# Kernel tuning notes

Measured on AMD Instinct MI355X. Metric: run time of the kernel, lower is better.

## Reference

```python
import jax, jax.numpy as jnp
import numpy as np
import math

B, N, M = 128, 32, 64           # batch, num_agents, num_other
OBS, ACT = 128, 16              # obs_input_dim, num_actions
D_QK = 128                      # obs_output_dim (== obs_output_dim_other)
D_AV = 64                       # obs_act_output_dim (== other)
F_IN = OBS + ACT                # obs_act_input_dim = 144


def _xavier(key, shape):
    fan_in, fan_out = shape[0], shape[1]
    limit = math.sqrt(6.0 / (fan_in + fan_out))
    return jax.random.uniform(key, shape, jnp.float32, -limit, limit)


def setup_inputs() -> dict:
    key = jax.random.key(0)
    ks = jax.random.split(key, 13)
    return {
        "states": jax.random.normal(ks[0], (B, N, OBS), jnp.float32),
        "policies": jax.random.uniform(ks[1], (B, N, ACT), jnp.float32),
        "actions": jax.random.uniform(ks[2], (B, N, ACT), jnp.float32),
        "states_other": jax.random.normal(ks[3], (B, M, OBS), jnp.float32),
        "actions_other": jax.random.uniform(ks[4], (B, M, ACT), jnp.float32),
        # weights stored as [in, out] (x @ W == nn.Linear without bias)
        "W_key": _xavier(ks[5], (OBS, D_QK)),
        "W_query": _xavier(ks[6], (OBS, D_QK)),
        "W_av": _xavier(ks[7], (F_IN, D_AV)),
        "W_key_other": _xavier(ks[8], (OBS, D_QK)),
        "W_query_other": _xavier(ks[9], (OBS, D_QK)),
        "W_av_other": _xavier(ks[10], (F_IN, D_AV)),
        "W_f1": _xavier(ks[11], (2 * D_AV, 64)),
        "W_f2": _xavier(ks[12], (64, 1)),
    }


def reference(states, policies, actions, states_other, actions_other,
              W_key, W_query, W_av, W_key_other, W_query_other,
              W_av_other, W_f1, W_f2):
    b, n, _ = states.shape
    obs_actions = jnp.concatenate([states, actions], axis=-1)   # [B,N,F_IN]
    obs_policy = jnp.concatenate([states, policies], axis=-1)   # [B,N,F_IN]

    key_obs = states @ W_key                                    # [B,N,D_QK]
    query_obs = states @ W_query                                # [B,N,D_QK]
    d_k = W_key.shape[1]
    weight = jax.nn.softmax(
        jnp.einsum('bid,bjd->bij', query_obs, key_obs) / math.sqrt(d_k), axis=-1)
    ret_weight = weight

    # place_policies is identity on (j,k): oap[b,j,k] = obs_policy[b,k] if j==k else obs_actions[b,k]
    eye = jnp.eye(n, dtype=states.dtype)[None, :, :, None]       # [1,N,N,1]
    oap = eye * obs_policy[:, None, :, :] + (1.0 - eye) * obs_actions[:, None, :, :]
    attention_values = jnp.tanh(oap @ W_av)                      # [B,N,N,D_AV] (j,k)

    # repeat-mul-sum == weighted reduction over k: wav[b,i,j,d] = sum_k w[b,i,k] av[b,j,k,d]
    wav = jnp.einsum('bik,bjkd->bijd', weight, attention_values)  # [B,N,N,D_AV]

    obs_actions_other = jnp.concatenate([states_other, actions_other], axis=-1)
    keys_other = states_other @ W_key_other                      # [B,M,D_QK]
    query_agent = states @ W_query_other                         # [B,N,D_QK]
    av_other = jnp.tanh(obs_actions_other @ W_av_other)          # [B,M,D_AV]
    d_k_o = W_key_other.shape[1]
    weight_other = jax.nn.softmax(
        jnp.einsum('bid,bmd->bim', query_agent, keys_other) / math.sqrt(d_k_o), axis=-1)
    wav_other = jnp.einsum('bim,bmd->bid', weight_other, av_other)  # [B,N,D_AV]

    # broadcast the per-agent other-branch features across the j axis for the concat
    wav_other_b = jnp.broadcast_to(wav_other[:, :, None, :], wav.shape[:-1] + (wav_other.shape[-1],))
    node_features = jnp.concatenate([wav, wav_other_b], axis=-1)  # [B,N,N,2*D_AV]

    h = jax.nn.leaky_relu(node_features @ W_f1, negative_slope=0.01)
    value = h @ W_f2                                              # [B,N,N,1]
    return value, ret_weight, weight_other
```

## Files before the change

kernel.cpp:

```cpp
#include <hip/hip_runtime.h>
#include <math.h>

#define WS_WQK    0
#define WS_WQKO   16384
#define WS_AVAPRJ 32768
#define WS_DPROJ  294912
#define WS_AVOPRJ 557056

#define INV_SQRT_DK 0.08838834764831845f

__device__ __forceinline__ float dot4(float4 a, float4 b) {
  return a.x*b.x + a.y*b.y + a.z*b.z + a.w*b.w;
}

__global__ __launch_bounds__(256) void k1_pre(
    const float* __restrict__ g_states, const float* __restrict__ g_pol,
    const float* __restrict__ g_act, const float* __restrict__ g_so,
    const float* __restrict__ g_ao,
    const float* __restrict__ Wq, const float* __restrict__ Wk,
    const float* __restrict__ Wqo, const float* __restrict__ Wko,
    const float* __restrict__ W_av, const float* __restrict__ W_avo,
    const float* __restrict__ W_f1, float* __restrict__ ws)
{
  __shared__ __align__(16) float pool[8576];
  const int t = threadIdx.x;
  int blk = blockIdx.x;

  if (blk < 32) {
    const float* A; const float* Bm; float* O;
    if (blk < 16) { A = Wq;  Bm = Wk;  O = ws + WS_WQK; }
    else          { A = Wqo; Bm = Wko; O = ws + WS_WQKO; blk -= 16; }
    const int tr = (blk >> 2) << 5;
    const int tc = (blk & 3) << 5;
    float* sA = pool;
    float* sB = pool + 4224;
    const float4* a4 = (const float4*)(A + tr * 128);
    const float4* b4 = (const float4*)(Bm + tc * 128);
    #pragma unroll
    for (int u = 0; u < 4; ++u) {
      int f = t + u * 256;
      int r = f >> 5, c4 = f & 31;
      *(float4*)(sA + r*132 + c4*4) = a4[f];
      *(float4*)(sB + r*132 + c4*4) = b4[f];
    }
    __syncthreads();
    const int e = t & 31, cl0 = t >> 5;
    float acc[4] = {0,0,0,0};
    #pragma unroll 4
    for (int d4 = 0; d4 < 32; ++d4) {
      float4 bv = *(const float4*)(sB + e*132 + d4*4);
      #pragma unroll
      for (int rr = 0; rr < 4; ++rr) {
        float4 av = *(const float4*)(sA + (cl0 + rr*8)*132 + d4*4);
        acc[rr] += dot4(av, bv);
      }
    }
    #pragma unroll
    for (int rr = 0; rr < 4; ++rr)
      O[(tr + cl0 + rr*8)*128 + tc + e] = acc[rr];
    return;
  }
  blk -= 32;

  if (blk < 128) {
    const int b = blk;
    float* s_pre = pool;
    float* s_av  = pool + 4224;
    float* s_dl  = pool + 6400;
    {
      const int wv_  = t >> 6;
      const int ap   = wv_ & 1;
      const int rh   = wv_ >> 1;
      const int lane = t & 63;
      const float* gs = g_states + b*4096 + rh*16*128;
      const float* gt = (ap ? g_pol : g_act) + b*512 + rh*16*16;
      float acc[16];
      #pragma unroll
      for (int r = 0; r < 16; ++r) acc[r] = 0.f;
      #pragma unroll 4
      for (int c4 = 0; c4 < 32; ++c4) {
        const float w0 = W_av[(c4*4+0)*64 + lane];
        const float w1 = W_av[(c4*4+1)*64 + lane];
        const float w2 = W_av[(c4*4+2)*64 + lane];
        const float w3 = W_av[(c4*4+3)*64 + lane];
        #pragma unroll
        for (int r = 0; r < 16; ++r) {
          float4 sv = *(const float4*)(gs + r*128 + c4*4);
          acc[r] += sv.x*w0 + sv.y*w1 + sv.z*w2 + sv.w*w3;
        }
      }
      #pragma unroll
      for (int c4 = 0; c4 < 4; ++c4) {
        const float w0 = W_av[(128 + c4*4+0)*64 + lane];
        const float w1 = W_av[(128 + c4*4+1)*64 + lane];
        const float w2 = W_av[(128 + c4*4+2)*64 + lane];
        const float w3 = W_av[(128 + c4*4+3)*64 + lane];
        #pragma unroll
        for (int r = 0; r < 16; ++r) {
          float4 sv = *(const float4*)(gt + r*16 + c4*4);
          acc[r] += sv.x*w0 + sv.y*w1 + sv.z*w2 + sv.w*w3;
        }
      }
      #pragma unroll
      for (int r = 0; r < 16; ++r)
        s_pre[(rh*16 + r)*132 + ap*64 + lane] = acc[r];
    }
    __syncthreads();
    {
      const int r = t >> 3, d0 = (t & 7) << 3;
      float4 a0 = *(const float4*)(s_pre + r*132 + d0);
      float4 a1 = *(const float4*)(s_pre + r*132 + d0 + 4);
      float4 p0 = *(const float4*)(s_pre + r*132 + 64 + d0);
      float4 p1 = *(const float4*)(s_pre + r*132 + 64 + d0 + 4);
      float4 va0, va1, dl0, dl1;
      va0.x = tanhf(a0.x); va0.y = tanhf(a0.y); va0.z = tanhf(a0.z); va0.w = tanhf(a0.w);
      va1.x = tanhf(a1.x); va1.y = tanhf(a1.y); va1.z = tanhf(a1.z); va1.w = tanhf(a1.w);
      dl0.x = tanhf(p0.x) - va0.x; dl0.y = tanhf(p0.y) - va0.y;
      dl0.z = tanhf(p0.z) - va0.z; dl0.w = tanhf(p0.w) - va0.w;
      dl1.x = tanhf(p1.x) - va1.x; dl1.y = tanhf(p1.y) - va1.y;
      dl1.z = tanhf(p1.z) - va1.z; dl1.w = tanhf(p1.w) - va1.w;
      *(float4*)(s_av + r*68 + d0)     = va0;
      *(float4*)(s_av + r*68 + d0 + 4) = va1;
      *(float4*)(s_dl + r*68 + d0)     = dl0;
      *(float4*)(s_dl + r*68 + d0 + 4) = dl1;
    }
    __syncthreads();
    {
      const int h = t & 63;
      const int j0 = (t >> 6) << 3;
      float da[8] = {0,0,0,0,0,0,0,0};
      float aa[8] = {0,0,0,0,0,0,0,0};
      #pragma unroll 4
      for (int d4 = 0; d4 < 16; ++d4) {
        float w0 = W_f1[(d4*4+0)*64 + h];
        float w1 = W_f1[(d4*4+1)*64 + h];
        float w2 = W_f1[(d4*4+2)*64 + h];
        float w3 = W_f1[(d4*4+3)*64 + h];
        #pragma unroll
        for (int q = 0; q < 8; ++q) {
          float4 dv = *(const float4*)(s_dl + (j0+q)*68 + d4*4);
          float4 av = *(const float4*)(s_av + (j0+q)*68 + d4*4);
          da[q] += dv.x*w0 + dv.y*w1 + dv.z*w2 + dv.w*w3;
          aa[q] += av.x*w0 + av.y*w1 + av.z*w2 + av.w*w3;
        }
      }
      #pragma unroll
      for (int q = 0; q < 8; ++q) {
        ws[WS_DPROJ  + b*2048 + (j0+q)*64 + h] = da[q];
        ws[WS_AVAPRJ + b*2048 + (j0+q)*64 + h] = aa[q];
      }
    }
    return;
  }
  blk -= 128;

  {
    const int b = blk >> 1, m0 = (blk & 1) << 5;
    float* s_avo = pool;
    const int wv_  = t >> 6;
    const int lane = t & 63;
    const float* gso = g_so + (b*64 + m0 + wv_*8) * 128;
    const float* gao = g_ao + (b*64 + m0 + wv_*8) * 16;
    float acc[8];
    #pragma unroll
    for (int r = 0; r < 8; ++r) acc[r] = 0.f;
    #pragma unroll 4
    for (int c4 = 0; c4 < 32; ++c4) {
      const float w0 = W_avo[(c4*4+0)*64 + lane];
      const float w1 = W_avo[(c4*4+1)*64 + lane];
      const float w2 = W_avo[(c4*4+2)*64 + lane];
      const float w3 = W_avo[(c4*4+3)*64 + lane];
      #pragma unroll
      for (int r = 0; r < 8; ++r) {
        float4 sv = *(const float4*)(gso + r*128 + c4*4);
        acc[r] += sv.x*w0 + sv.y*w1 + sv.z*w2 + sv.w*w3;
      }
    }
    #pragma unroll
    for (int c4 = 0; c4 < 4; ++c4) {
      const float w0 = W_avo[(128 + c4*4+0)*64 + lane];
      const float w1 = W_avo[(128 + c4*4+1)*64 + lane];
      const float w2 = W_avo[(128 + c4*4+2)*64 + lane];
      const float w3 = W_avo[(128 + c4*4+3)*64 + lane];
      #pragma unroll
      for (int r = 0; r < 8; ++r) {
        float4 sv = *(const float4*)(gao + r*16 + c4*4);
        acc[r] += sv.x*w0 + sv.y*w1 + sv.z*w2 + sv.w*w3;
      }
    }
    #pragma unroll
    for (int r = 0; r < 8; ++r)
      s_avo[(wv_*8 + r)*68 + lane] = tanhf(acc[r]);
    __syncthreads();
    {
      const int h = t & 63;
      const int j0 = (t >> 6) << 3;
      float oa[8] = {0,0,0,0,0,0,0,0};
      #pragma unroll 4
      for (int d4 = 0; d4 < 16; ++d4) {
        float w0 = W_f1[(64 + d4*4+0)*64 + h];
        float w1 = W_f1[(64 + d4*4+1)*64 + h];
        float w2 = W_f1[(64 + d4*4+2)*64 + h];
        float w3 = W_f1[(64 + d4*4+3)*64 + h];
        #pragma unroll
        for (int q = 0; q < 8; ++q) {
          float4 ov = *(const float4*)(s_avo + (j0+q)*68 + d4*4);
          oa[q] += ov.x*w0 + ov.y*w1 + ov.z*w2 + ov.w*w3;
        }
      }
      #pragma unroll
      for (int q = 0; q < 8; ++q)
        ws[WS_AVOPRJ + b*4096 + (m0 + j0 + q)*64 + h] = oa[q];
    }
  }
}

__global__ __launch_bounds__(256) void k2_main(
    const float* __restrict__ g_states, const float* __restrict__ g_so,
    const float* __restrict__ ws, float* __restrict__ out,
    const float* __restrict__ W_f2)
{
  __shared__ __align__(16) float pool[12288];
  float* s_st   = pool;
  float* s_avOp = pool;
  float* s_avAp = pool + 4352;
  float* s_dp   = pool + 6528;
  float* s_P    = pool + 8704;
  float* s_w    = pool + 10848;
  float* s_wo   = pool + 11136;
  float* s_base = pool + 11680;
  float* s_wf2  = pool + 12224;

  const int t = threadIdx.x;
  const int b = blockIdx.x >> 2;
  const int i0 = (blockIdx.x & 3) << 3;

  {
    const float4* gs4 = (const float4*)(g_states + b * 4096);
    #pragma unroll
    for (int u = 0; u < 4; ++u) {
      int f = t + u * 256;
      int r = f >> 5, c4 = f & 31;
      *(float4*)(s_st + r*132 + c4*4) = gs4[f];
    }
    #pragma unroll
    for (int u = 0; u < 2; ++u) {
      int f = t + u * 256;
      int k = f >> 4, dq = f & 15;
      *(float4*)(s_avAp + k*68 + dq*4) = ((const float4*)(ws + WS_AVAPRJ + b*2048))[f];
      *(float4*)(s_dp   + k*68 + dq*4) = ((const float4*)(ws + WS_DPROJ  + b*2048))[f];
    }
    if (t < 16) *(float4*)(s_wf2 + t*4) = ((const float4*)W_f2)[t];
  }

  {
    const int wv_ = t >> 6, lane = t & 63;
    const int cg  = wv_*64 + lane;
    const float* Wp = (wv_ < 2) ? (ws + WS_WQK  + cg)
                                : (ws + WS_WQKO + cg - 128);
    const float* srow = g_states + b*4096 + i0*128;
    float acc[8] = {0,0,0,0,0,0,0,0};
    #pragma unroll 4
    for (int c4 = 0; c4 < 32; ++c4) {
      float4 sv[8];
      #pragma unroll
      for (int r = 0; r < 8; ++r)
        sv[r] = *(const float4*)(srow + r*128 + c4*4);
      #pragma unroll
      for (int kk = 0; kk < 4; ++kk) {
        float wv = Wp[(c4*4 + kk)*128];
        #pragma unroll
        for (int r = 0; r < 8; ++r)
          acc[r] += wv * ((const float*)&sv[r])[kk];
      }
    }
    #pragma unroll
    for (int r = 0; r < 8; ++r)
      s_P[r*268 + cg] = acc[r];
  }
  __syncthreads();

  {
    const int r = t >> 5, j = t & 31;
    float acc = 0.f;
    #pragma unroll 8
    for (int e4 = 0; e4 < 32; ++e4) {
      float4 p4  = *(const float4*)(s_P + r*268 + e4*4);
      float4 st4 = *(const float4*)(s_st + j*132 + e4*4);
      acc += dot4(p4, st4);
    }
    acc *= INV_SQRT_DK;
    float mx = acc;
    for (int off = 16; off; off >>= 1) mx = fmaxf(mx, __shfl_xor(mx, off, 32));
    float ev = __expf(acc - mx);
    float sum = ev;
    for (int off = 16; off; off >>= 1) sum += __shfl_xor(sum, off, 32);
    float wn = ev / sum;
    out[131072 + b*1024 + (i0 + r)*32 + j] = wn;
    s_w[r*36 + j] = wn;
  }
  __syncthreads();

  for (int tt = 0; tt < 2; ++tt) {
    const float4* gt4 = (const float4*)(g_so + (b*64 + tt*32) * 128);
    #pragma unroll
    for (int u = 0; u < 4; ++u) {
      int f = t + u * 256;
      int r = f >> 5, c4 = f & 31;
      *(float4*)(s_st + r*132 + c4*4) = gt4[f];
    }
    __syncthreads();
    const int r = t >> 5, m = t & 31;
    float acc = 0.f;
    #pragma unroll 8
    for (int c4 = 0; c4 < 32; ++c4) {
      float4 p4  = *(const float4*)(s_P + r*268 + 128 + c4*4);
      float4 st4 = *(const float4*)(s_st + m*132 + c4*4);
      acc += dot4(p4, st4);
    }
    s_wo[r*68 + tt*32 + m] = acc * INV_SQRT_DK;
    __syncthreads();
  }

  #pragma unroll
  for (int p = 0; p < 2; ++p) {
    const int r = (t >> 6) + (p << 2), l = t & 63;
    float v = s_wo[r*68 + l];
    float mx = v;
    for (int off = 32; off; off >>= 1) mx = fmaxf(mx, __shfl_xor(mx, off, 64));
    float ev = __expf(v - mx);
    float sum = ev;
    for (int off = 32; off; off >>= 1) sum += __shfl_xor(sum, off, 64);
    float wn = ev / sum;
    out[262144 + b*2048 + (i0 + r)*64 + l] = wn;
    s_wo[r*68 + l] = wn;
  }
  #pragma unroll
  for (int u = 0; u < 4; ++u) {
    int f = t + u * 256;
    int m = f >> 4, dq = f & 15;
    *(float4*)(s_avOp + m*68 + dq*4) = ((const float4*)(ws + WS_AVOPRJ + b*4096))[f];
  }
  __syncthreads();

  {
    const int g = t >> 6, h = t & 63;
    const int r0 = g*2, r1 = r0 + 1;
    float a0 = 0.f, a1 = 0.f;
    #pragma unroll 2
    for (int k4 = 0; k4 < 8; ++k4) {
      float4 wa = *(const float4*)(s_w + r0*36 + k4*4);
      float4 wb = *(const float4*)(s_w + r1*36 + k4*4);
      #pragma unroll
      for (int kk = 0; kk < 4; ++kk) {
        float pv = s_avAp[(k4*4 + kk)*68 + h];
        a0 += ((const float*)&wa)[kk] * pv;
        a1 += ((const float*)&wb)[kk] * pv;
      }
    }
    #pragma unroll 2
    for (int m4 = 0; m4 < 16; ++m4) {
      float4 wa = *(const float4*)(s_wo + r0*68 + m4*4);
      float4 wb = *(const float4*)(s_wo + r1*68 + m4*4);
      #pragma unroll
      for (int kk = 0; kk < 4; ++kk) {
        float pv = s_avOp[(m4*4 + kk)*68 + h];
        a0 += ((const float*)&wa)[kk] * pv;
        a1 += ((const float*)&wb)[kk] * pv;
      }
    }
    s_base[r0*68 + h] = a0;
    s_base[r1*68 + h] = a1;
  }
  __syncthreads();

  {
    const int i = t >> 5, j = t & 31;
    const float wij = s_w[i*36 + j];
    float acc = 0.f;
    #pragma unroll 4
    for (int hq = 0; hq < 16; ++hq) {
      float4 b4 = *(const float4*)(s_base + i*68 + hq*4);
      float4 d4 = *(const float4*)(s_dp + j*68 + hq*4);
      float4 f4 = *(const float4*)(s_wf2 + hq*4);
      float p0 = b4.x + wij*d4.x; p0 = p0 > 0.f ? p0 : 0.01f*p0;
      float p1 = b4.y + wij*d4.y; p1 = p1 > 0.f ? p1 : 0.01f*p1;
      float p2 = b4.z + wij*d4.z; p2 = p2 > 0.f ? p2 : 0.01f*p2;
      float p3 = b4.w + wij*d4.w; p3 = p3 > 0.f ? p3 : 0.01f*p3;
      acc += p0*f4.x + p1*f4.y + p2*f4.z + p3*f4.w;
    }
    out[b*1024 + (i0 + i)*32 + j] = acc;
  }
}

extern "C" void kernel_launch(void* const* d_in, const int* in_sizes, int n_in,
                              void* d_out, int out_size, void* d_ws, size_t ws_size,
                              hipStream_t stream) {
  const float* states        = (const float*)d_in[0];
  const float* policies      = (const float*)d_in[1];
  const float* actions       = (const float*)d_in[2];
  const float* states_other  = (const float*)d_in[3];
  const float* actions_other = (const float*)d_in[4];
  const float* W_key         = (const float*)d_in[5];
  const float* W_query       = (const float*)d_in[6];
  const float* W_av          = (const float*)d_in[7];
  const float* W_key_other   = (const float*)d_in[8];
  const float* W_query_other = (const float*)d_in[9];
  const float* W_av_other    = (const float*)d_in[10];
  const float* W_f1          = (const float*)d_in[11];
  const float* W_f2          = (const float*)d_in[12];
  float* out = (float*)d_out;
  float* ws  = (float*)d_ws;

  k1_pre<<<416, 256, 0, stream>>>(states, policies, actions, states_other,
                                  actions_other, W_query, W_key,
                                  W_query_other, W_key_other, W_av, W_av_other,
                                  W_f1, ws);
  k2_main<<<512, 256, 0, stream>>>(states, states_other, ws, out, W_f2);
}
```

Baseline: 132.3 us.

## Stage intermediates through global memory instead of LDS and cut shared usage

After: 190.8 us. +44.2%, slower.

```diff
diff --git a/kernel.cpp b/kernel.cpp
--- a/kernel.cpp
+++ b/kernel.cpp
@@ -1,11 +1,14 @@
 #include <hip/hip_runtime.h>
 #include <math.h>
 
-#define WS_WQK    0
-#define WS_WQKO   16384
-#define WS_AVAPRJ 32768
-#define WS_DPROJ  294912
-#define WS_AVOPRJ 557056
+#define WS_WQK     0
+#define WS_WQKO    16384
+#define WS_AVA     32768
+#define WS_DELTA   294912
+#define WS_AVO     557056
+#define WS_AVAPRJ  1081344
+#define WS_DPROJ   1343488
+#define WS_AVOPRJ  1605632
 
 #define INV_SQRT_DK 0.08838834764831845f
 
@@ -13,7 +16,7 @@
   return a.x*b.x + a.y*b.y + a.z*b.z + a.w*b.w;
 }
 
-__global__ __launch_bounds__(256) void k1_pre(
+__global__ __launch_bounds__(256, 4) void k1_pre(
     const float* __restrict__ g_states, const float* __restrict__ g_pol,
     const float* __restrict__ g_act, const float* __restrict__ g_so,
     const float* __restrict__ g_ao,
@@ -22,7 +25,7 @@
     const float* __restrict__ W_av, const float* __restrict__ W_avo,
     const float* __restrict__ W_f1, float* __restrict__ ws)
 {
-  __shared__ __align__(16) float pool[8576];
+  __shared__ __align__(16) float pool[8448];
   const int t = threadIdx.x;
   int blk = blockIdx.x;
 
@@ -64,19 +67,12 @@
 
   if (blk < 128) {
     const int b = blk;
-    float* s_pre = pool;
-    float* s_av  = pool + 4224;
-    float* s_dl  = pool + 6400;
+    const int rg = t >> 6, lane = t & 63;
     {
-      const int wv_  = t >> 6;
-      const int ap   = wv_ & 1;
-      const int rh   = wv_ >> 1;
-      const int lane = t & 63;
-      const float* gs = g_states + b*4096 + rh*16*128;
-      const float* gt = (ap ? g_pol : g_act) + b*512 + rh*16*16;
-      float acc[16];
-      #pragma unroll
-      for (int r = 0; r < 16; ++r) acc[r] = 0.f;
+      const float* gs = g_states + b*4096 + rg*8*128;
+      const float* ga = g_act + b*512 + rg*8*16;
+      const float* gp = g_pol + b*512 + rg*8*16;
+      float accS[8] = {0,0,0,0,0,0,0,0};
       #pragma unroll 4
       for (int c4 = 0; c4 < 32; ++c4) {
         const float w0 = W_av[(c4*4+0)*64 + lane];
@@ -84,11 +80,14 @@
         const float w2 = W_av[(c4*4+2)*64 + lane];
         const float w3 = W_av[(c4*4+3)*64 + lane];
         #pragma unroll
-        for (int r = 0; r < 16; ++r) {
+        for (int r = 0; r < 8; ++r) {
           float4 sv = *(const float4*)(gs + r*128 + c4*4);
-          acc[r] += sv.x*w0 + sv.y*w1 + sv.z*w2 + sv.w*w3;
-        }
-      }
+          accS[r] += sv.x*w0 + sv.y*w1 + sv.z*w2 + sv.w*w3;
+        }
+      }
+      float accA[8], accP[8];
+      #pragma unroll
+      for (int r = 0; r < 8; ++r) { accA[r] = accS[r]; accP[r] = accS[r]; }
       #pragma unroll
       for (int c4 = 0; c4 < 4; ++c4) {
         const float w0 = W_av[(128 + c4*4+0)*64 + lane];
@@ -96,168 +95,131 @@
         const float w2 = W_av[(128 + c4*4+2)*64 + lane];
         const float w3 = W_av[(128 + c4*4+3)*64 + lane];
         #pragma unroll
-        for (int r = 0; r < 16; ++r) {
-          float4 sv = *(const float4*)(gt + r*16 + c4*4);
-          acc[r] += sv.x*w0 + sv.y*w1 + sv.z*w2 + sv.w*w3;
-        }
-      }
-      #pragma unroll
-      for (int r = 0; r < 16; ++r)
-        s_pre[(rh*16 + r)*132 + ap*64 + lane] = acc[r];
+        for (int r = 0; r < 8; ++r) {
+          float4 sa = *(const float4*)(ga + r*16 + c4*4);
+          float4 sp = *(const float4*)(gp + r*16 + c4*4);
+          accA[r] += sa.x*w0 + sa.y*w1 + sa.z*w2 + sa.w*w3;
+          accP[r] += sp.x*w0 + sp.y*w1 + sp.z*w2 + sp.w*w3;
+        }
+      }
+      #pragma unroll
+      for (int r = 0; r < 8; ++r) {
+        float va = tanhf(accA[r]);
+        float dl = tanhf(accP[r]) - va;
+        ws[WS_AVA   + b*2048 + (rg*8 + r)*64 + lane] = va;
+        ws[WS_DELTA + b*2048 + (rg*8 + r)*64 + lane] = dl;
+      }
     }
     __syncthreads();
     {
-      const int r = t >> 3, d0 = (t & 7) << 3;
-      float4 a0 = *(const float4*)(s_pre + r*132 + d0);
-      float4 a1 = *(const float4*)(s_pre + r*132 + d0 + 4);
-      float4 p0 = *(const float4*)(s_pre + r*132 + 64 + d0);
-      float4 p1 = *(const float4*)(s_pre + r*132 + 64 + d0 + 4);
-      float4 va0, va1, dl0, dl1;
-      va0.x = tanhf(a0.x); va0.y = tanhf(a0.y); va0.z = tanhf(a0.z); va0.w = tanhf(a0.w);
-      va1.x = tanhf(a1.x); va1.y = tanhf(a1.y); va1.z = tanhf(a1.z); va1.w = tanhf(a1.w);
-      dl0.x = tanhf(p0.x) - va0.x; dl0.y = tanhf(p0.y) - va0.y;
-      dl0.z = tanhf(p0.z) - va0.z; dl0.w = tanhf(p0.w) - va0.w;
-      dl1.x = tanhf(p1.x) - va1.x; dl1.y = tanhf(p1.y) - va1.y;
-      dl1.z = tanhf(p1.z) - va1.z; dl1.w = tanhf(p1.w) - va1.w;
-      *(float4*)(s_av + r*68 + d0)     = va0;
-      *(float4*)(s_av + r*68 + d0 + 4) = va1;
-      *(float4*)(s_dl + r*68 + d0)     = dl0;
-      *(float4*)(s_dl + r*68 + d0 + 4) = dl1;
+      const int arr = rg & 1, j0 = (rg >> 1) * 16;
+      const float* src = ws + (arr ? WS_DELTA : WS_AVA) + b*2048 + j0*64;
+      float*       dst = ws + (arr ? WS_DPROJ : WS_AVAPRJ) + b*2048 + j0*64;
+      float acc[16];
+      #pragma unroll
+      for (int q = 0; q < 16; ++q) acc[q] = 0.f;
+      #pragma unroll 2
+      for (int d4 = 0; d4 < 16; ++d4) {
+        const float w0 = W_f1[(d4*4+0)*64 + lane];
+        const float w1 = W_f1[(d4*4+1)*64 + lane];
+        const float w2 = W_f1[(d4*4+2)*64 + lane];
+        const float w3 = W_f1[(d4*4+3)*64 + lane];
+        #pragma unroll
+        for (int q = 0; q < 16; ++q) {
+          float4 dv = *(const float4*)(src + q*64 + d4*4);
+          acc[q] += dv.x*w0 + dv.y*w1 + dv.z*w2 + dv.w*w3;
+        }
+      }
+      #pragma unroll
+      for (int q = 0; q < 16; ++q)
+        dst[q*64 + lane] = acc[q];
+    }
+    return;
+  }
+  blk -= 128;
+
+  {
+    const int b = blk >> 1, m0 = (blk & 1) << 5;
+    const int rg = t >> 6, lane = t & 63;
+    {
+      const float* gso = g_so + (b*64 + m0 + rg*8) * 128;
+      const float* gao = g_ao + (b*64 + m0 + rg*8) * 16;
+      float acc[8] = {0,0,0,0,0,0,0,0};
+      #pragma unroll 4
+      for (int c4 = 0; c4 < 32; ++c4) {
+        const float w0 = W_avo[(c4*4+0)*64 + lane];
+        const float w1 = W_avo[(c4*4+1)*64 + lane];
+        const float w2 = W_avo[(c4*4+2)*64 + lane];
+        const float w3 = W_avo[(c4*4+3)*64 + lane];
+        #pragma unroll
+        for (int r = 0; r < 8; ++r) {
+          float4 sv = *(const float4*)(gso + r*128 + c4*4);
+          acc[r] += sv.x*w0 + sv.y*w1 + sv.z*w2 + sv.w*w3;
+        }
+      }
+      #pragma unroll
+      for (int c4 = 0; c4 < 4; ++c4) {
+        const float w0 = W_avo[(128 + c4*4+0)*64 + lane];
+        const float w1 = W_avo[(128 + c4*4+1)*64 + lane];
+        const float w2 = W_avo[(128 + c4*4+2)*64 + lane];
+        const float w3 = W_avo[(128 + c4*4+3)*64 + lane];
+        #pragma unroll
+        for (int r = 0; r < 8; ++r) {
+          float4 sv = *(const float4*)(gao + r*16 + c4*4);
+          acc[r] += sv.x*w0 + sv.y*w1 + sv.z*w2 + sv.w*w3;
+        }
+      }
+      #pragma unroll
+      for (int r = 0; r < 8; ++r)
+        ws[WS_AVO + b*4096 + (m0 + rg*8 + r)*64 + lane] = tanhf(acc[r]);
     }
     __syncthreads();
     {
-      const int h = t & 63;
-      const int j0 = (t >> 6) << 3;
-      float da[8] = {0,0,0,0,0,0,0,0};
-      float aa[8] = {0,0,0,0,0,0,0,0};
-      #pragma unroll 4
+      const int j0 = m0 + rg*8;
+      const float* src = ws + WS_AVO + b*4096 + j0*64;
+      float*       dst = ws + WS_AVOPRJ + b*4096 + j0*64;
+      float acc[8] = {0,0,0,0,0,0,0,0};
+      #pragma unroll 2
       for (int d4 = 0; d4 < 16; ++d4) {
-        float w0 = W_f1[(d4*4+0)*64 + h];
-        float w1 = W_f1[(d4*4+1)*64 + h];
-        float w2 = W_f1[(d4*4+2)*64 + h];
-        float w3 = W_f1[(d4*4+3)*64 + h];
+        const float w0 = W_f1[(64 + d4*4+0)*64 + lane];
+        const float w1 = W_f1[(64 + d4*4+1)*64 + lane];
+        const float w2 = W_f1[(64 + d4*4+2)*64 + lane];
+        const float w3 = W_f1[(64 + d4*4+3)*64 + lane];
         #pragma unroll
         for (int q = 0; q < 8; ++q) {
-          float4 dv = *(const float4*)(s_dl + (j0+q)*68 + d4*4);
-          float4 av = *(const float4*)(s_av + (j0+q)*68 + d4*4);
-          da[q] += dv.x*w0 + dv.y*w1 + dv.z*w2 + dv.w*w3;
-          aa[q] += av.x*w0 + av.y*w1 + av.z*w2 + av.w*w3;
-        }
-      }
-      #pragma unroll
-      for (int q = 0; q < 8; ++q) {
-        ws[WS_DPROJ  + b*2048 + (j0+q)*64 + h] = da[q];
-        ws[WS_AVAPRJ + b*2048 + (j0+q)*64 + h] = aa[q];
-      }
-    }
-    return;
-  }
-  blk -= 128;
-
-  {
-    const int b = blk >> 1, m0 = (blk & 1) << 5;
-    float* s_avo = pool;
-    const int wv_  = t >> 6;
-    const int lane = t & 63;
-    const float* gso = g_so + (b*64 + m0 + wv_*8) * 128;
-    const float* gao = g_ao + (b*64 + m0 + wv_*8) * 16;
-    float acc[8];
-    #pragma unroll
-    for (int r = 0; r < 8; ++r) acc[r] = 0.f;
-    #pragma unroll 4
-    for (int c4 = 0; c4 < 32; ++c4) {
-      const float w0 = W_avo[(c4*4+0)*64 + lane];
-      const float w1 = W_avo[(c4*4+1)*64 + lane];
-      const float w2 = W_avo[(c4*4+2)*64 + lane];
-      const float w3 = W_avo[(c4*4+3)*64 + lane];
-      #pragma unroll
-      for (int r = 0; r < 8; ++r) {
-        float4 sv = *(const float4*)(gso + r*128 + c4*4);
-        acc[r] += sv.x*w0 + sv.y*w1 + sv.z*w2 + sv.w*w3;
-      }
-    }
-    #pragma unroll
-    for (int c4 = 0; c4 < 4; ++c4) {
-      const float w0 = W_avo[(128 + c4*4+0)*64 + lane];
-      const float w1 = W_avo[(128 + c4*4+1)*64 + lane];
-      const float w2 = W_avo[(128 + c4*4+2)*64 + lane];
-      const float w3 = W_avo[(128 + c4*4+3)*64 + lane];
-      #pragma unroll
-      for (int r = 0; r < 8; ++r) {
-        float4 sv = *(const float4*)(gao + r*16 + c4*4);
-        acc[r] += sv.x*w0 + sv.y*w1 + sv.z*w2 + sv.w*w3;
-      }
-    }
-    #pragma unroll
-    for (int r = 0; r < 8; ++r)
-      s_avo[(wv_*8 + r)*68 + lane] = tanhf(acc[r]);
-    __syncthreads();
-    {
-      const int h = t & 63;
-      const int j0 = (t >> 6) << 3;
-      float oa[8] = {0,0,0,0,0,0,0,0};
-      #pragma unroll 4
-      for (int d4 = 0; d4 < 16; ++d4) {
-        float w0 = W_f1[(64 + d4*4+0)*64 + h];
-        float w1 = W_f1[(64 + d4*4+1)*64 + h];
-        float w2 = W_f1[(64 + d4*4+2)*64 + h];
-        float w3 = W_f1[(64 + d4*4+3)*64 + h];
-        #pragma unroll
-        for (int q = 0; q < 8; ++q) {
-          float4 ov = *(const float4*)(s_avo + (j0+q)*68 + d4*4);
-          oa[q] += ov.x*w0 + ov.y*w1 + ov.z*w2 + ov.w*w3;
+          float4 ov = *(const float4*)(src + q*64 + d4*4);
+          acc[q] += ov.x*w0 + ov.y*w1 + ov.z*w2 + ov.w*w3;
         }
       }
       #pragma unroll
       for (int q = 0; q < 8; ++q)
-        ws[WS_AVOPRJ + b*4096 + (m0 + j0 + q)*64 + h] = oa[q];
+        dst[q*64 + lane] = acc[q];
     }
   }
 }
 
-__global__ __launch_bounds__(256) void k2_main(
+__global__ __launch_bounds__(256, 4) void k2_main(
     const float* __restrict__ g_states, const float* __restrict__ g_so,
     const float* __restrict__ ws, float* __restrict__ out,
     const float* __restrict__ W_f2)
 {
-  __shared__ __align__(16) float pool[12288];
-  float* s_st   = pool;
-  float* s_avOp = pool;
-  float* s_avAp = pool + 4352;
-  float* s_dp   = pool + 6528;
-  float* s_P    = pool + 8704;
-  float* s_w    = pool + 10848;
-  float* s_wo   = pool + 11136;
-  float* s_base = pool + 11680;
-  float* s_wf2  = pool + 12224;
+  __shared__ __align__(16) float s_P[8*268];
+  __shared__ __align__(16) float s_w[8*36];
+  __shared__ __align__(16) float s_wo[8*68];
+  __shared__ __align__(16) float s_base[8*68];
+  __shared__ __align__(16) float s_wf2[64];
 
   const int t = threadIdx.x;
   const int b = blockIdx.x >> 2;
   const int i0 = (blockIdx.x & 3) << 3;
 
-  {
-    const float4* gs4 = (const float4*)(g_states + b * 4096);
-    #pragma unroll
-    for (int u = 0; u < 4; ++u) {
-      int f = t + u * 256;
-      int r = f >> 5, c4 = f & 31;
-      *(float4*)(s_st + r*132 + c4*4) = gs4[f];
-    }
-    #pragma unroll
-    for (int u = 0; u < 2; ++u) {
-      int f = t + u * 256;
-      int k = f >> 4, dq = f & 15;
-      *(float4*)(s_avAp + k*68 + dq*4) = ((const float4*)(ws + WS_AVAPRJ + b*2048))[f];
-      *(float4*)(s_dp   + k*68 + dq*4) = ((const float4*)(ws + WS_DPROJ  + b*2048))[f];
-    }
-    if (t < 16) *(float4*)(s_wf2 + t*4) = ((const float4*)W_f2)[t];
-  }
-
-  {
-    const int wv_ = t >> 6, lane = t & 63;
-    const int cg  = wv_*64 + lane;
-    const float* Wp = (wv_ < 2) ? (ws + WS_WQK  + cg)
-                                : (ws + WS_WQKO + cg - 128);
+  if (t < 16) *(float4*)(s_wf2 + t*4) = ((const float4*)W_f2)[t];
+
+  {
+    const int wv = t >> 6, lane = t & 63;
+    const int cg = wv*64 + lane;
+    const float* Wp = (wv < 2) ? (ws + WS_WQK  + cg)
+                               : (ws + WS_WQKO + cg - 128);
     const float* srow = g_states + b*4096 + i0*128;
     float acc[8] = {0,0,0,0,0,0,0,0};
     #pragma unroll 4
@@ -268,10 +230,10 @@
         sv[r] = *(const float4*)(srow + r*128 + c4*4);
       #pragma unroll
       for (int kk = 0; kk < 4; ++kk) {
-        float wv = Wp[(c4*4 + kk)*128];
+        float wvv = Wp[(c4*4 + kk)*128];
         #pragma unroll
         for (int r = 0; r < 8; ++r)
-          acc[r] += wv * ((const float*)&sv[r])[kk];
+          acc[r] += wvv * ((const float*)&sv[r])[kk];
       }
     }
     #pragma unroll
@@ -286,7 +248,7 @@
     #pragma unroll 8
     for (int e4 = 0; e4 < 32; ++e4) {
       float4 p4  = *(const float4*)(s_P + r*268 + e4*4);
-      float4 st4 = *(const float4*)(s_st + j*132 + e4*4);
+      float4 st4 = *(const float4*)(g_states + b*4096 + j*128 + e4*4);
       acc += dot4(p4, st4);
     }
     acc *= INV_SQRT_DK;
@@ -298,29 +260,20 @@
     float wn = ev / sum;
     out[131072 + b*1024 + (i0 + r)*32 + j] = wn;
     s_w[r*36 + j] = wn;
+
+    #pragma unroll
+    for (int tt = 0; tt < 2; ++tt) {
+      float a2 = 0.f;
+      #pragma unroll 8
+      for (int c4 = 0; c4 < 32; ++c4) {
+        float4 p4  = *(const float4*)(s_P + r*268 + 128 + c4*4);
+        float4 so4 = *(const float4*)(g_so + (b*64 + tt*32 + j)*128 + c4*4);
+        a2 += dot4(p4, so4);
+      }
+      s_wo[r*68 + tt*32 + j] = a2 * INV_SQRT_DK;
+    }
   }
   __syncthreads();
-
-  for (int tt = 0; tt < 2; ++tt) {
-    const float4* gt4 = (const float4*)(g_so + (b*64 + tt*32) * 128);
-    #pragma unroll
-    for (int u = 0; u < 4; ++u) {
-      int f = t + u * 256;
-      int r = f >> 5, c4 = f & 31;
-      *(float4*)(s_st + r*132 + c4*4) = gt4[f];
-    }
-    __syncthreads();
-    const int r = t >> 5, m = t & 31;
-    float acc = 0.f;
-    #pragma unroll 8
-    for (int c4 = 0; c4 < 32; ++c4) {
-      float4 p4  = *(const float4*)(s_P + r*268 + 128 + c4*4);
-      float4 st4 = *(const float4*)(s_st + m*132 + c4*4);
-      acc += dot4(p4, st4);
-    }
-    s_wo[r*68 + tt*32 + m] = acc * INV_SQRT_DK;
-    __syncthreads();
-  }
 
   #pragma unroll
   for (int p = 0; p < 2; ++p) {
@@ -335,17 +288,13 @@
     out[262144 + b*2048 + (i0 + r)*64 + l] = wn;
     s_wo[r*68 + l] = wn;
   }
-  #pragma unroll
-  for (int u = 0; u < 4; ++u) {
-    int f = t + u * 256;
-    int m = f >> 4, dq = f & 15;
-    *(float4*)(s_avOp + m*68 + dq*4) = ((const float4*)(ws + WS_AVOPRJ + b*4096))[f];
-  }
   __syncthreads();
 
   {
     const int g = t >> 6, h = t & 63;
     const int r0 = g*2, r1 = r0 + 1;
+    const float* ap_ = ws + WS_AVAPRJ + b*2048 + h;
+    const float* op_ = ws + WS_AVOPRJ + b*4096 + h;
     float a0 = 0.f, a1 = 0.f;
     #pragma unroll 2
     for (int k4 = 0; k4 < 8; ++k4) {
@@ -353,7 +302,7 @@
       float4 wb = *(const float4*)(s_w + r1*36 + k4*4);
       #pragma unroll
       for (int kk = 0; kk < 4; ++kk) {
-        float pv = s_avAp[(k4*4 + kk)*68 + h];
+        float pv = ap_[(k4*4 + kk)*64];
         a0 += ((const float*)&wa)[kk] * pv;
         a1 += ((const float*)&wb)[kk] * pv;
       }
@@ -364,7 +313,7 @@
       float4 wb = *(const float4*)(s_wo + r1*68 + m4*4);
       #pragma unroll
       for (int kk = 0; kk < 4; ++kk) {
-        float pv = s_avOp[(m4*4 + kk)*68 + h];
+        float pv = op_[(m4*4 + kk)*64];
         a0 += ((const float*)&wa)[kk] * pv;
         a1 += ((const float*)&wb)[kk] * pv;
       }
@@ -377,11 +326,12 @@
   {
     const int i = t >> 5, j = t & 31;
     const float wij = s_w[i*36 + j];
+    const float* dp = ws + WS_DPROJ + b*2048 + j*64;
     float acc = 0.f;
     #pragma unroll 4
     for (int hq = 0; hq < 16; ++hq) {
       float4 b4 = *(const float4*)(s_base + i*68 + hq*4);
-      float4 d4 = *(const float4*)(s_dp + j*68 + hq*4);
+      float4 d4 = *(const float4*)(dp + hq*4);
       float4 f4 = *(const float4*)(s_wf2 + hq*4);
       float p0 = b4.x + wij*d4.x; p0 = p0 > 0.f ? p0 : 0.01f*p0;
       float p1 = b4.y + wij*d4.y; p1 = p1 > 0.f ? p1 : 0.01f*p1;
```
